# Kernel optimization log

Measured on AMD Instinct MI355X. Metric: run time of the kernel, lower is better.

The kernel has to match this reference:

```python
import jax, jax.numpy as jnp
import numpy as np

B, L, C = 4, 8192, 256
HEADS = 1
DP = C // HEADS
FFN_HID = C * 2 * 4  # (d_model*2) * ffn_dim_expansion
EPS = 1e-5


def _layernorm(x, gamma, beta):
    mu = jnp.mean(x, axis=-1, keepdims=True)
    var = jnp.var(x, axis=-1, keepdims=True)
    return (x - mu) * jax.lax.rsqrt(var + EPS) * gamma + beta


def setup_inputs() -> dict:
    key = jax.random.key(0)
    ks = jax.random.split(key, 12)
    s = 0.02
    return {
        "source": jax.random.normal(ks[0], (B, L, C), jnp.float32),
        "target": jax.random.normal(ks[1], (B, L, C), jnp.float32),
        "Wq": jax.random.normal(ks[2], (C, C), jnp.float32) * s,
        "Wk": jax.random.normal(ks[3], (C, C), jnp.float32) * s,
        "Wv": jax.random.normal(ks[4], (C, C), jnp.float32) * s,
        "Wl": jax.random.normal(ks[5], (C, C), jnp.float32) * s,
        "gamma1": jnp.ones((C,), jnp.float32),
        "beta1": jnp.zeros((C,), jnp.float32),
        "W1": jax.random.normal(ks[6], (2 * C, FFN_HID), jnp.float32) * s,
        "b1": jnp.zeros((FFN_HID,), jnp.float32),
        "W2": jax.random.normal(ks[7], (FFN_HID, C), jnp.float32) * s,
        "b2": jnp.zeros((C,), jnp.float32),
        "gamma2": jnp.ones((C,), jnp.float32),
        "beta2": jnp.zeros((C,), jnp.float32),
        "h": 64,
        "w": 128,
    }


def reference(source, target, Wq, Wk, Wv, Wl, gamma1, beta1, W1, b1, W2, b2,
              gamma2, beta2, h, w):
    assert L == h * w
    q = (source @ Wq).reshape(B, L, HEADS, DP)
    k = (target @ Wk).reshape(B, L, HEADS, DP)
    v = (target @ Wv).reshape(B, L, HEADS, DP)
    k = jax.nn.softmax(k, axis=1)  # softmax over token dim
    context = jnp.einsum('bnhd,bnhe->bhde', q, k)   # small d×d per head
    attn = jnp.einsum('bhde,bnhe->bnhd', context, v).reshape(B, L, C)
    message = _layernorm(attn @ Wl, gamma1, beta1)
    hidden = jax.nn.gelu(jnp.concatenate([source, message], axis=-1) @ W1 + b1,
                         approximate=False)
    message = _layernorm(hidden @ W2 + b2, gamma2, beta2)
    return source + message
```

## Files before the change

kernel.cpp:

```cpp
#include <hip/hip_runtime.h>
#include <hip/hip_bf16.h>

typedef unsigned short u16;
typedef __attribute__((ext_vector_type(8))) short short8;
typedef __attribute__((ext_vector_type(4))) float f32x4;

#define B_    4
#define L_    8192
#define C_    256
#define BL_   (B_*L_)
#define BLC_  (BL_*C_)
#define FFN_  2048
#define KCAT_ 512
#define EPS_  1e-5f

__device__ __forceinline__ float bf2f(u16 v) {
  union { unsigned int u; float f; } x; x.u = ((unsigned int)v) << 16; return x.f;
}
__device__ __forceinline__ u16 f2bf(float f) {
  union { float f; unsigned int u; } x; x.f = f;
  unsigned int lsb = (x.u >> 16) & 1u;
  return (u16)((x.u + 0x7fffu + lsb) >> 16);
}
__device__ __forceinline__ float gelu_f(float x) {
  float z = fabsf(x) * 0.70710678118654752f;
  float t = __builtin_amdgcn_rcpf(1.f + 0.3275911f * z);
  float p = ((((1.061405429f * t - 1.453152027f) * t + 1.421413741f) * t
              - 0.284496736f) * t + 0.254829592f) * t;
  float e = __expf(-z * z);
  float erfv = copysignf(1.f - p * e, x);
  return 0.5f * x * (1.f + erfv);
}

template<int MODE, int ACT, int SPLITK>
__launch_bounds__(256, 2)
__global__ void gemm_abt(const u16* __restrict__ A0, const u16* __restrict__ A1,
                         int SEL, int lda,
                         const u16* __restrict__ Bt,
                         const float* __restrict__ bias,
                         u16* __restrict__ Cb, float* __restrict__ Cf,
                         int M, int N, int K,
                         long sAb, long sBb, long sCb)
{
  __shared__ __align__(16) u16 As[2 * 128 * 32];
  __shared__ __align__(16) u16 Bs[2 * 128 * 32];

  const int ntiles = N >> 7;
  const int tile = blockIdx.x;
  const int mt0 = (tile / ntiles) << 7;
  const int nt0 = (tile % ntiles) << 7;
  const int kchunk = K / (int)gridDim.y;
  const int k0beg = blockIdx.y * kchunk;
  const int k0end = k0beg + kchunk;
  const int bz = blockIdx.z;
  A0 += (long)bz * sAb;  A1 += (long)bz * sAb;  Bt += (long)bz * sBb;

  const u16* Abase = (MODE == 2 && nt0 >= SEL) ? A1 : A0;

  const int tid  = threadIdx.x;
  const int wave = tid >> 6, lane = tid & 63;
  const int srow = lane >> 2;
  const int cq   = lane & 3;
  const int gq   = cq ^ (srow & 3);
  const int frow = lane & 15;
  const int fq   = lane >> 4;
  const int fqx  = (fq ^ (frow & 3)) * 8;

  f32x4 zero = {0.f, 0.f, 0.f, 0.f};
  f32x4 acc[4][4];
#pragma unroll
  for (int i = 0; i < 4; i++)
#pragma unroll
    for (int j = 0; j < 4; j++) acc[i][j] = zero;

  const int wm = (wave & 1) * 64, wn = (wave >> 1) * 64;

  for (int k0 = k0beg; k0 < k0end; k0 += 64) {
    __syncthreads();
    const u16* Asrc;
    int ka;
    if (MODE == 1) {
      const bool lo = (k0 < SEL);
      Asrc = lo ? A0 : A1;
      ka = lo ? k0 : (k0 - SEL);
    } else { Asrc = Abase; ka = k0; }

#pragma unroll
    for (int h = 0; h < 2; h++) {
#pragma unroll
      for (int i = 0; i < 2; i++) {
        const int chunk = i * 4 + wave;
        const u16* ga = Asrc + (long)(mt0 + chunk * 16 + srow) * lda
                        + (ka + h * 32 + gq * 8);
        __builtin_amdgcn_global_load_lds(
            (const __attribute__((address_space(1))) unsigned int*)ga,
            (__attribute__((address_space(3))) unsigned int*)&As[h * 4096 + chunk * 16 * 32],
            16, 0, 0);
        const u16* gb = Bt + (long)(nt0 + chunk * 16 + srow) * K
                        + (k0 + h * 32 + gq * 8);
        __builtin_amdgcn_global_load_lds(
            (const __attribute__((address_space(1))) unsigned int*)gb,
            (__attribute__((address_space(3))) unsigned int*)&Bs[h * 4096 + chunk * 16 * 32],
            16, 0, 0);
      }
    }
    __syncthreads();

#pragma unroll
    for (int h = 0; h < 2; h++) {
      short8 af[4], bf[4];
#pragma unroll
      for (int t = 0; t < 4; t++)
        af[t] = *(const short8*)&As[h * 4096 + (wm + t * 16 + frow) * 32 + fqx];
#pragma unroll
      for (int t = 0; t < 4; t++)
        bf[t] = *(const short8*)&Bs[h * 4096 + (wn + t * 16 + frow) * 32 + fqx];
#pragma unroll
      for (int mt = 0; mt < 4; mt++)
#pragma unroll
        for (int nt = 0; nt < 4; nt++)
          acc[mt][nt] = __builtin_amdgcn_mfma_f32_16x16x32_bf16(af[mt], bf[nt], acc[mt][nt], 0, 0, 0);
    }
  }

  if (SPLITK) {
    float* Cp = Cf + (long)bz * sCb;
#pragma unroll
    for (int mt = 0; mt < 4; mt++)
#pragma unroll
      for (int r = 0; r < 4; r++) {
        const int row = mt0 + wm + mt * 16 + fq * 4 + r;
#pragma unroll
        for (int nt = 0; nt < 4; nt++) {
          const int col = nt0 + wn + nt * 16 + frow;
          atomicAdd(&Cp[(long)row * N + col], acc[mt][nt][r]);
        }
      }
  } else {
    u16* Cp = Cb + (long)bz * sCb;
    float bv[4];
#pragma unroll
    for (int nt = 0; nt < 4; nt++)
      bv[nt] = bias ? bias[nt0 + wn + nt * 16 + frow] : 0.f;
#pragma unroll
    for (int mt = 0; mt < 4; mt++)
#pragma unroll
      for (int r = 0; r < 4; r++) {
        const int row = mt0 + wm + mt * 16 + fq * 4 + r;
#pragma unroll
        for (int nt = 0; nt < 4; nt++) {
          const int col = nt0 + wn + nt * 16 + frow;
          float v = acc[mt][nt][r] + bv[nt];
          if (ACT == 1) v = gelu_f(v);
          Cp[(long)row * N + col] = f2bf(v);
        }
      }
  }
}

__global__ void transpose2d(const u16* __restrict__ in, u16* __restrict__ out,
                            int R, int Cc, int ldi, long sIb, long sOb)
{
  __shared__ u16 t[32][33];
  const int bx = blockIdx.x * 32;
  const int by = blockIdx.y * 32;
  in  += (long)blockIdx.z * sIb;
  out += (long)blockIdx.z * sOb;
  const int tx = threadIdx.x, ty = threadIdx.y;
#pragma unroll
  for (int i = ty; i < 32; i += 8)
    t[i][tx] = in[(long)(by + i) * ldi + bx + tx];
  __syncthreads();
#pragma unroll
  for (int i = ty; i < 32; i += 8)
    out[(long)(bx + i) * R + by + tx] = t[tx][i];
}

__global__ void transpose_f2b(const float* __restrict__ in, u16* __restrict__ out,
                              int R, int Cc)
{
  __shared__ u16 t[32][33];
  const int bx = blockIdx.x * 32;
  const int by = blockIdx.y * 32;
  const int tx = threadIdx.x, ty = threadIdx.y;
#pragma unroll
  for (int i = ty; i < 32; i += 8)
    t[i][tx] = f2bf(in[(long)(by + i) * Cc + bx + tx]);
  __syncthreads();
#pragma unroll
  for (int i = ty; i < 32; i += 8)
    out[(long)(bx + i) * R + by + tx] = t[tx][i];
}

__global__ void pack_w256(const float* __restrict__ w0, const float* __restrict__ w1,
                          const float* __restrict__ w2, const float* __restrict__ w3,
                          u16* __restrict__ qkvT, u16* __restrict__ wlT)
{
  __shared__ u16 t[32][33];
  const int z = blockIdx.z;
  const float* in = (z == 0) ? w0 : (z == 1) ? w1 : (z == 2) ? w2 : w3;
  u16* out = (z < 3) ? (qkvT + (long)z * C_ * C_) : wlT;
  const int bx = blockIdx.x * 32, by = blockIdx.y * 32;
  const int tx = threadIdx.x, ty = threadIdx.y;
#pragma unroll
  for (int i = ty; i < 32; i += 8)
    t[i][tx] = f2bf(in[(long)(by + i) * C_ + bx + tx]);
  __syncthreads();
#pragma unroll
  for (int i = ty; i < 32; i += 8)
    out[(long)(bx + i) * C_ + by + tx] = t[tx][i];
}

__global__ void cast2_f2b(const float* __restrict__ in0, const float* __restrict__ in1,
                          u16* __restrict__ out0, u16* __restrict__ out1)
{
  const float* in = blockIdx.y ? in1 : in0;
  u16* out = blockIdx.y ? out1 : out0;
  int i = (blockIdx.x * 256 + threadIdx.x) * 4;
  float4 v = *(const float4*)(in + i);
  ushort4 o; o.x = f2bf(v.x); o.y = f2bf(v.y); o.z = f2bf(v.z); o.w = f2bf(v.w);
  *(ushort4*)(out + i) = o;
}

__global__ void softmax_rows(u16* __restrict__ data, int rowlen)
{
  const long base = (long)blockIdx.x * rowlen;
  const int tid = threadIdx.x, wave = tid >> 6, lane = tid & 63;
  __shared__ float red[4];

  float m = -3.4e38f;
  for (int i = tid; i < rowlen; i += 256) m = fmaxf(m, bf2f(data[base + i]));
#pragma unroll
  for (int off = 32; off; off >>= 1) m = fmaxf(m, __shfl_xor(m, off, 64));
  if (lane == 0) red[wave] = m;
  __syncthreads();
  m = fmaxf(fmaxf(red[0], red[1]), fmaxf(red[2], red[3]));
  __syncthreads();

  float s = 0.f;
  for (int i = tid; i < rowlen; i += 256) s += expf(bf2f(data[base + i]) - m);
#pragma unroll
  for (int off = 32; off; off >>= 1) s += __shfl_xor(s, off, 64);
  if (lane == 0) red[wave] = s;
  __syncthreads();
  const float inv = 1.f / (red[0] + red[1] + red[2] + red[3]);
  for (int i = tid; i < rowlen; i += 256)
    data[base + i] = f2bf(expf(bf2f(data[base + i]) - m) * inv);
}

template<int OUTF>
__global__ void layernorm_rows(const u16* __restrict__ x,
                               const float* __restrict__ gamma,
                               const float* __restrict__ beta,
                               const float* __restrict__ src,
                               void* __restrict__ outv)
{
  const int wave = threadIdx.x >> 6, lane = threadIdx.x & 63;
  const long row = (long)blockIdx.x * 4 + wave;
  ushort4 raw = ((const ushort4*)(x + row * C_))[lane];
  float v0 = bf2f(raw.x), v1 = bf2f(raw.y), v2 = bf2f(raw.z), v3 = bf2f(raw.w);
  float s = v0 + v1 + v2 + v3;
  float q = v0 * v0 + v1 * v1 + v2 * v2 + v3 * v3;
#pragma unroll
  for (int off = 32; off; off >>= 1) {
    s += __shfl_xor(s, off, 64);
    q += __shfl_xor(q, off, 64);
  }
  const float mu  = s * (1.f / C_);
  const float var = q * (1.f / C_) - mu * mu;
  const float rs  = 1.f / sqrtf(var + EPS_);
  float4 gr = ((const float4*)gamma)[lane];
  float4 br = ((const float4*)beta)[lane];
  float o0 = (v0 - mu) * rs * gr.x + br.x;
  float o1 = (v1 - mu) * rs * gr.y + br.y;
  float o2 = (v2 - mu) * rs * gr.z + br.z;
  float o3 = (v3 - mu) * rs * gr.w + br.w;
  if (OUTF) {
    float4 sr = ((const float4*)(src + row * C_))[lane];
    float4 ow; ow.x = o0 + sr.x; ow.y = o1 + sr.y; ow.z = o2 + sr.z; ow.w = o3 + sr.w;
    ((float4*)((float*)outv + row * C_))[lane] = ow;
  } else {
    ushort4 ow; ow.x = f2bf(o0); ow.y = f2bf(o1); ow.z = f2bf(o2); ow.w = f2bf(o3);
    ((ushort4*)((u16*)outv + row * C_))[lane] = ow;
  }
}

__global__ void zero_f32(float* __restrict__ p, int n) {
  int i = blockIdx.x * 256 + threadIdx.x;
  if (i < n) p[i] = 0.f;
}
__global__ void f32_to_bf16_k(const float* __restrict__ in, u16* __restrict__ out, int n) {
  int i = blockIdx.x * 256 + threadIdx.x;
  if (i < n) out[i] = f2bf(in[i]);
}

extern "C" void kernel_launch(void* const* d_in, const int* in_sizes, int n_in,
                              void* d_out, int out_size, void* d_ws, size_t ws_size,
                              hipStream_t stream)
{
  const float* source = (const float*)d_in[0];
  const float* target = (const float*)d_in[1];
  const float* Wq     = (const float*)d_in[2];
  const float* Wk     = (const float*)d_in[3];
  const float* Wv     = (const float*)d_in[4];
  const float* Wl     = (const float*)d_in[5];
  const float* gamma1 = (const float*)d_in[6];
  const float* beta1  = (const float*)d_in[7];
  const float* W1     = (const float*)d_in[8];
  const float* b1     = (const float*)d_in[9];
  const float* W2     = (const float*)d_in[10];
  const float* b2     = (const float*)d_in[11];
  const float* gamma2 = (const float*)d_in[12];
  const float* beta2  = (const float*)d_in[13];
  (void)in_sizes; (void)n_in; (void)out_size;

  char* ws = (char*)d_ws;
  size_t off = 0;
  auto take = [&](size_t bytes) -> char* {
    char* p = ws + off; off += (bytes + 255) & ~(size_t)255; return p;
  };
  u16*   WqkvT = (u16*)take((size_t)768 * C_ * 2);
  u16*   WlT   = (u16*)take((size_t)C_ * C_ * 2);
  u16*   W1T   = (u16*)take((size_t)FFN_ * KCAT_ * 2);
  u16*   W2T   = (u16*)take((size_t)C_ * FFN_ * 2);
  float* ctxTf = (float*)take((size_t)B_ * C_ * C_ * 4);
  u16*   ctxTb = (u16*)take((size_t)B_ * C_ * C_ * 2);
  u16*   Mtb   = (u16*)take((size_t)B_ * C_ * C_ * 2);
  u16*   srcB  = (u16*)take((size_t)BLC_ * 2);
  u16*   bufB  = (u16*)take((size_t)BLC_ * 2);
  u16*   bufD  = (u16*)take((size_t)BLC_ * 2);
  u16*   bufE  = (u16*)take((size_t)BLC_ * 2);
  const size_t ubase = off;
  u16* tgtB = (u16*)(ws + ubase);
  u16* QKV  = (u16*)(ws + ubase + (size_t)BLC_ * 2);
  u16* qT   = (u16*)(ws + ubase + (size_t)BLC_ * 2 + (size_t)BL_ * 768 * 2);
  u16* kT   = qT + (size_t)BLC_;
  const size_t live = (size_t)BLC_ * 2 * 3 + (size_t)BL_ * 768 * 2;
  int nchunk = 1;
  while (nchunk < 16) {
    size_t hid = (size_t)(BL_ / nchunk) * FFN_ * 2;
    size_t need = ubase + (hid > live ? hid : live);
    if (need <= ws_size) break;
    nchunk <<= 1;
  }
  const int Mc = BL_ / nchunk;
  u16* hidden = (u16*)(ws + ubase);

  dim3 tb(32, 8);
  cast2_f2b<<<dim3(BLC_ / 1024, 2), 256, 0, stream>>>(source, target, srcB, tgtB);
  pack_w256<<<dim3(8, 8, 4), tb, 0, stream>>>(Wq, Wk, Wv, Wl, WqkvT, WlT);
  transpose_f2b<<<dim3(FFN_/32, KCAT_/32), tb, 0, stream>>>(W1, W1T, KCAT_, FFN_);
  transpose_f2b<<<dim3(C_/32,  FFN_/32), tb, 0, stream>>>(W2, W2T, FFN_, C_);
  zero_f32<<<(B_*C_*C_)/256, 256, 0, stream>>>(ctxTf, B_*C_*C_);

  gemm_abt<2,0,0><<<dim3((BL_/128)*(768/128)), 256, 0, stream>>>(
      srcB, tgtB, 256, C_, WqkvT, nullptr, QKV, nullptr, BL_, 768, C_, 0, 0, 0);

  transpose2d<<<dim3(C_/32, L_/32, B_), tb, 0, stream>>>(QKV,       qT, L_, C_, 768, (long)L_*768, (long)L_*C_);
  transpose2d<<<dim3(C_/32, L_/32, B_), tb, 0, stream>>>(QKV + 256, kT, L_, C_, 768, (long)L_*768, (long)L_*C_);
  softmax_rows<<<B_*C_, 256, 0, stream>>>(kT, L_);

  gemm_abt<0,0,1><<<dim3(4, 16, B_), 256, 0, stream>>>(
      kT, kT, 0, L_, qT, nullptr, nullptr, ctxTf, C_, C_, L_,
      (long)C_*L_, (long)C_*L_, (long)C_*C_);
  f32_to_bf16_k<<<(B_*C_*C_)/256, 256, 0, stream>>>(ctxTf, ctxTb, B_*C_*C_);

  gemm_abt<0,0,0><<<dim3(4, 1, B_), 256, 0, stream>>>(
      WlT, WlT, 0, C_, ctxTb, nullptr, Mtb, nullptr, C_, C_, C_,
      0, (long)C_*C_, (long)C_*C_);

  gemm_abt<0,0,0><<<dim3((L_/128)*(C_/128), 1, B_), 256, 0, stream>>>(
      QKV + 512, QKV + 512, 0, 768, Mtb, nullptr, bufB, nullptr, L_, C_, C_,
      (long)L_*768, (long)C_*C_, (long)L_*C_);

  layernorm_rows<0><<<BL_/4, 256, 0, stream>>>(bufB, gamma1, beta1, nullptr, bufD);

  for (int ch = 0; ch < nchunk; ch++) {
    const long moff = (long)ch * Mc;
    gemm_abt<1,1,0><<<dim3((Mc/128)*(FFN_/128)), 256, 0, stream>>>(
        srcB + moff * C_, bufD + moff * C_, C_, C_, W1T, b1, hidden, nullptr,
        Mc, FFN_, KCAT_, 0, 0, 0);
    gemm_abt<0,0,0><<<dim3((Mc/128)*(C_/128)), 256, 0, stream>>>(
        hidden, hidden, 0, FFN_, W2T, b2, bufE + moff * C_, nullptr,
        Mc, C_, FFN_, 0, 0, 0);
  }

  layernorm_rows<1><<<BL_/4, 256, 0, stream>>>(bufE, gamma2, beta2, source, d_out);
}
```

Before: 420.3 us.

## Fuse attention-out GEMM with LayerNorm and fuse whole FFN into one kernel

Replaces the attn@Wl GEMM plus separate LayerNorm with a gemm_ln kernel that computes 64x256 row tiles and applies LayerNorm in the epilogue. The two FFN GEMMs, GELU, bias, LayerNorm2 and the residual add move into one ffn_fused kernel that keeps the hidden activations in LDS per 128-column slice, so the large hidden buffer never goes through HBM. This removes the intermediate memory traffic and several launches. The cost is lower tile reuse with 64-row tiles, many more synchronisations, and W1/W2 being reread for every row block. The generic GEMM also switches to M-major tile ordering.

```diff
diff --git a/kernel.cpp b/kernel.cpp
--- a/kernel.cpp
+++ b/kernel.cpp
@@ -14,6 +14,10 @@
 #define KCAT_ 512
 #define EPS_  1e-5f
 
+#define GLDS(dst, src) __builtin_amdgcn_global_load_lds( \
+    (const __attribute__((address_space(1))) unsigned int*)(src), \
+    (__attribute__((address_space(3))) unsigned int*)(dst), 16, 0, 0)
+
 __device__ __forceinline__ float bf2f(u16 v) {
   union { unsigned int u; float f; } x; x.u = ((unsigned int)v) << 16; return x.f;
 }
@@ -32,12 +36,11 @@
   return 0.5f * x * (1.f + erfv);
 }
 
-template<int MODE, int ACT, int SPLITK>
+template<int MODE, int SPLITK>
 __launch_bounds__(256, 2)
 __global__ void gemm_abt(const u16* __restrict__ A0, const u16* __restrict__ A1,
                          int SEL, int lda,
                          const u16* __restrict__ Bt,
-                         const float* __restrict__ bias,
                          u16* __restrict__ Cb, float* __restrict__ Cf,
                          int M, int N, int K,
                          long sAb, long sBb, long sCb)
@@ -45,10 +48,10 @@
   __shared__ __align__(16) u16 As[2 * 128 * 32];
   __shared__ __align__(16) u16 Bs[2 * 128 * 32];
 
-  const int ntiles = N >> 7;
+  const int mtiles = M >> 7;
   const int tile = blockIdx.x;
-  const int mt0 = (tile / ntiles) << 7;
-  const int nt0 = (tile % ntiles) << 7;
+  const int mt0 = (tile % mtiles) << 7;
+  const int nt0 = (tile / mtiles) << 7;
   const int kchunk = K / (int)gridDim.y;
   const int k0beg = blockIdx.y * kchunk;
   const int k0end = k0beg + kchunk;
@@ -60,8 +63,7 @@
   const int tid  = threadIdx.x;
   const int wave = tid >> 6, lane = tid & 63;
   const int srow = lane >> 2;
-  const int cq   = lane & 3;
-  const int gq   = cq ^ (srow & 3);
+  const int gq   = (lane & 3) ^ (srow & 3);
   const int frow = lane & 15;
   const int fq   = lane >> 4;
   const int fqx  = (fq ^ (frow & 3)) * 8;
@@ -77,35 +79,18 @@
 
   for (int k0 = k0beg; k0 < k0end; k0 += 64) {
     __syncthreads();
-    const u16* Asrc;
-    int ka;
-    if (MODE == 1) {
-      const bool lo = (k0 < SEL);
-      Asrc = lo ? A0 : A1;
-      ka = lo ? k0 : (k0 - SEL);
-    } else { Asrc = Abase; ka = k0; }
-
 #pragma unroll
     for (int h = 0; h < 2; h++) {
 #pragma unroll
       for (int i = 0; i < 2; i++) {
         const int chunk = i * 4 + wave;
-        const u16* ga = Asrc + (long)(mt0 + chunk * 16 + srow) * lda
-                        + (ka + h * 32 + gq * 8);
-        __builtin_amdgcn_global_load_lds(
-            (const __attribute__((address_space(1))) unsigned int*)ga,
-            (__attribute__((address_space(3))) unsigned int*)&As[h * 4096 + chunk * 16 * 32],
-            16, 0, 0);
-        const u16* gb = Bt + (long)(nt0 + chunk * 16 + srow) * K
-                        + (k0 + h * 32 + gq * 8);
-        __builtin_amdgcn_global_load_lds(
-            (const __attribute__((address_space(1))) unsigned int*)gb,
-            (__attribute__((address_space(3))) unsigned int*)&Bs[h * 4096 + chunk * 16 * 32],
-            16, 0, 0);
+        GLDS(&As[h * 4096 + chunk * 512],
+             Abase + (long)(mt0 + chunk * 16 + srow) * lda + (k0 + h * 32 + gq * 8));
+        GLDS(&Bs[h * 4096 + chunk * 512],
+             Bt + (long)(nt0 + chunk * 16 + srow) * K + (k0 + h * 32 + gq * 8));
       }
     }
     __syncthreads();
-
 #pragma unroll
     for (int h = 0; h < 2; h++) {
       short8 af[4], bf[4];
@@ -131,39 +116,292 @@
       for (int r = 0; r < 4; r++) {
         const int row = mt0 + wm + mt * 16 + fq * 4 + r;
 #pragma unroll
-        for (int nt = 0; nt < 4; nt++) {
-          const int col = nt0 + wn + nt * 16 + frow;
-          atomicAdd(&Cp[(long)row * N + col], acc[mt][nt][r]);
-        }
+        for (int nt = 0; nt < 4; nt++)
+          atomicAdd(&Cp[(long)row * N + nt0 + wn + nt * 16 + frow], acc[mt][nt][r]);
       }
   } else {
     u16* Cp = Cb + (long)bz * sCb;
-    float bv[4];
-#pragma unroll
-    for (int nt = 0; nt < 4; nt++)
-      bv[nt] = bias ? bias[nt0 + wn + nt * 16 + frow] : 0.f;
 #pragma unroll
     for (int mt = 0; mt < 4; mt++)
 #pragma unroll
       for (int r = 0; r < 4; r++) {
         const int row = mt0 + wm + mt * 16 + fq * 4 + r;
 #pragma unroll
-        for (int nt = 0; nt < 4; nt++) {
-          const int col = nt0 + wn + nt * 16 + frow;
-          float v = acc[mt][nt][r] + bv[nt];
-          if (ACT == 1) v = gelu_f(v);
-          Cp[(long)row * N + col] = f2bf(v);
+        for (int nt = 0; nt < 4; nt++)
+          Cp[(long)row * N + nt0 + wn + nt * 16 + frow] = f2bf(acc[mt][nt][r]);
+      }
+  }
+}
+
+__launch_bounds__(256, 2)
+__global__ void gemm_ln(const u16* __restrict__ A, long sAb, int lda,
+                        const u16* __restrict__ Bt, long sBb,
+                        const float* __restrict__ gamma, const float* __restrict__ beta,
+                        u16* __restrict__ outb)
+{
+  __shared__ __align__(16) u16 As[2 * 64 * 32];
+  __shared__ __align__(16) u16 Bs[2 * 256 * 32];
+  __shared__ float red_s[64][4], red_q[64][4];
+
+  const int gm0 = blockIdx.x * 64;
+  const int z  = gm0 >> 13;
+  const int ml = gm0 & (L_ - 1);
+  A  += (long)z * sAb + (long)ml * lda;
+  Bt += (long)z * sBb;
+
+  const int tid = threadIdx.x, wave = tid >> 6, lane = tid & 63;
+  const int srow = lane >> 2, gq = (lane & 3) ^ (srow & 3);
+  const int frow = lane & 15, fq = lane >> 4;
+  const int fqx = (fq ^ (frow & 3)) * 8;
+  const int wn = wave * 64;
+
+  f32x4 zero = {0.f, 0.f, 0.f, 0.f};
+  f32x4 acc[4][4];
+#pragma unroll
+  for (int i = 0; i < 4; i++)
+#pragma unroll
+    for (int j = 0; j < 4; j++) acc[i][j] = zero;
+
+  for (int k0 = 0; k0 < 256; k0 += 64) {
+    __syncthreads();
+#pragma unroll
+    for (int h = 0; h < 2; h++) {
+      GLDS(&As[h * 2048 + wave * 512],
+           A + (long)(wave * 16 + srow) * lda + (k0 + h * 32 + gq * 8));
+#pragma unroll
+      for (int i = 0; i < 4; i++) {
+        const int chunk = i * 4 + wave;
+        GLDS(&Bs[h * 8192 + chunk * 512],
+             Bt + (long)(chunk * 16 + srow) * 256 + (k0 + h * 32 + gq * 8));
+      }
+    }
+    __syncthreads();
+#pragma unroll
+    for (int h = 0; h < 2; h++) {
+      short8 af[4], bf[4];
+#pragma unroll
+      for (int t = 0; t < 4; t++)
+        af[t] = *(const short8*)&As[h * 2048 + (t * 16 + frow) * 32 + fqx];
+#pragma unroll
+      for (int t = 0; t < 4; t++)
+        bf[t] = *(const short8*)&Bs[h * 8192 + (wn + t * 16 + frow) * 32 + fqx];
+#pragma unroll
+      for (int mt = 0; mt < 4; mt++)
+#pragma unroll
+        for (int nt = 0; nt < 4; nt++)
+          acc[mt][nt] = __builtin_amdgcn_mfma_f32_16x16x32_bf16(af[mt], bf[nt], acc[mt][nt], 0, 0, 0);
+    }
+  }
+
+  float gv[4], bv[4];
+#pragma unroll
+  for (int nt = 0; nt < 4; nt++) {
+    const int col = wn + nt * 16 + frow;
+    gv[nt] = gamma[col]; bv[nt] = beta[col];
+  }
+#pragma unroll
+  for (int mt = 0; mt < 4; mt++)
+#pragma unroll
+    for (int r = 0; r < 4; r++) {
+      float s = 0.f, q = 0.f;
+#pragma unroll
+      for (int nt = 0; nt < 4; nt++) {
+        float v = acc[mt][nt][r]; s += v; q += v * v;
+      }
+#pragma unroll
+      for (int m = 1; m < 16; m <<= 1) {
+        s += __shfl_xor(s, m, 16); q += __shfl_xor(q, m, 16);
+      }
+      if (frow == 0) {
+        const int row = mt * 16 + fq * 4 + r;
+        red_s[row][wave] = s; red_q[row][wave] = q;
+      }
+    }
+  __syncthreads();
+#pragma unroll
+  for (int mt = 0; mt < 4; mt++)
+#pragma unroll
+    for (int r = 0; r < 4; r++) {
+      const int row = mt * 16 + fq * 4 + r;
+      float4 ss = *(const float4*)red_s[row];
+      float4 qq = *(const float4*)red_q[row];
+      const float s = ss.x + ss.y + ss.z + ss.w;
+      const float q = qq.x + qq.y + qq.z + qq.w;
+      const float mu = s * (1.f / 256.f);
+      const float var = q * (1.f / 256.f) - mu * mu;
+      const float rs = 1.f / sqrtf(var + EPS_);
+      const long grow = gm0 + row;
+#pragma unroll
+      for (int nt = 0; nt < 4; nt++) {
+        const int col = wn + nt * 16 + frow;
+        outb[grow * 256 + col] = f2bf((acc[mt][nt][r] - mu) * rs * gv[nt] + bv[nt]);
+      }
+    }
+}
+
+__launch_bounds__(256, 2)
+__global__ void ffn_fused(const u16* __restrict__ srcB, const u16* __restrict__ message,
+                          const u16* __restrict__ W1T, const float* __restrict__ b1,
+                          const u16* __restrict__ W2T, const float* __restrict__ b2,
+                          const float* __restrict__ gamma2, const float* __restrict__ beta2,
+                          const float* __restrict__ source, float* __restrict__ out)
+{
+  __shared__ __align__(16) u16 As[2 * 64 * 32];
+  __shared__ __align__(16) u16 Bs1[2 * 128 * 32];
+  __shared__ __align__(16) u16 Bs2[2 * 256 * 32];
+  __shared__ __align__(16) u16 Hs[64 * 136];
+  __shared__ float red_s[64][4], red_q[64][4];
+
+  const int m0 = blockIdx.x * 64;
+  const int tid = threadIdx.x, wave = tid >> 6, lane = tid & 63;
+  const int srow = lane >> 2, gq = (lane & 3) ^ (srow & 3);
+  const int frow = lane & 15, fq = lane >> 4;
+  const int fqx = (fq ^ (frow & 3)) * 8;
+  const int wn1 = wave * 32;
+  const int wn2 = wave * 64;
+
+  f32x4 zero = {0.f, 0.f, 0.f, 0.f};
+  f32x4 acc2[4][4];
+#pragma unroll
+  for (int i = 0; i < 4; i++)
+#pragma unroll
+    for (int j = 0; j < 4; j++) acc2[i][j] = zero;
+
+  for (int hs = 0; hs < 16; hs++) {
+    f32x4 acc1[4][2];
+#pragma unroll
+    for (int i = 0; i < 4; i++) { acc1[i][0] = zero; acc1[i][1] = zero; }
+
+    for (int it = 0; it < 8; it++) {
+      const int k0 = it * 64;
+      const u16* Asrc = (k0 < 256) ? srcB : message;
+      const int ka = k0 & 255;
+      __syncthreads();
+#pragma unroll
+      for (int h = 0; h < 2; h++) {
+        GLDS(&As[h * 2048 + wave * 512],
+             Asrc + (long)(m0 + wave * 16 + srow) * 256 + (ka + h * 32 + gq * 8));
+#pragma unroll
+        for (int i = 0; i < 2; i++) {
+          const int chunk = i * 4 + wave;
+          GLDS(&Bs1[h * 4096 + chunk * 512],
+               W1T + (long)(hs * 128 + chunk * 16 + srow) * 512 + (k0 + h * 32 + gq * 8));
         }
       }
+      __syncthreads();
+#pragma unroll
+      for (int h = 0; h < 2; h++) {
+        short8 af[4], bf[2];
+#pragma unroll
+        for (int t = 0; t < 4; t++)
+          af[t] = *(const short8*)&As[h * 2048 + (t * 16 + frow) * 32 + fqx];
+#pragma unroll
+        for (int t = 0; t < 2; t++)
+          bf[t] = *(const short8*)&Bs1[h * 4096 + (wn1 + t * 16 + frow) * 32 + fqx];
+#pragma unroll
+        for (int mt = 0; mt < 4; mt++)
+#pragma unroll
+          for (int nt = 0; nt < 2; nt++)
+            acc1[mt][nt] = __builtin_amdgcn_mfma_f32_16x16x32_bf16(af[mt], bf[nt], acc1[mt][nt], 0, 0, 0);
+      }
+    }
+    float b1v[2];
+#pragma unroll
+    for (int nt = 0; nt < 2; nt++)
+      b1v[nt] = b1[hs * 128 + wn1 + nt * 16 + frow];
+#pragma unroll
+    for (int mt = 0; mt < 4; mt++)
+#pragma unroll
+      for (int nt = 0; nt < 2; nt++)
+#pragma unroll
+        for (int r = 0; r < 4; r++) {
+          const int row = mt * 16 + fq * 4 + r;
+          Hs[row * 136 + wn1 + nt * 16 + frow] = f2bf(gelu_f(acc1[mt][nt][r] + b1v[nt]));
+        }
+
+    for (int it2 = 0; it2 < 2; it2++) {
+      __syncthreads();
+#pragma unroll
+      for (int h = 0; h < 2; h++)
+#pragma unroll
+        for (int i = 0; i < 4; i++) {
+          const int chunk = i * 4 + wave;
+          GLDS(&Bs2[h * 8192 + chunk * 512],
+               W2T + (long)(chunk * 16 + srow) * 2048
+                   + (hs * 128 + it2 * 64 + h * 32 + gq * 8));
+        }
+      __syncthreads();
+#pragma unroll
+      for (int kk = 0; kk < 2; kk++) {
+        short8 a2[4], b2f[4];
+#pragma unroll
+        for (int t = 0; t < 4; t++)
+          a2[t] = *(const short8*)&Hs[(t * 16 + frow) * 136 + it2 * 64 + kk * 32 + fq * 8];
+#pragma unroll
+        for (int t = 0; t < 4; t++)
+          b2f[t] = *(const short8*)&Bs2[kk * 8192 + (wn2 + t * 16 + frow) * 32 + fqx];
+#pragma unroll
+        for (int mt = 0; mt < 4; mt++)
+#pragma unroll
+          for (int nt = 0; nt < 4; nt++)
+            acc2[mt][nt] = __builtin_amdgcn_mfma_f32_16x16x32_bf16(a2[mt], b2f[nt], acc2[mt][nt], 0, 0, 0);
+      }
+    }
   }
+
+  float b2v[4], gv[4], bv[4];
+#pragma unroll
+  for (int nt = 0; nt < 4; nt++) {
+    const int col = wn2 + nt * 16 + frow;
+    b2v[nt] = b2[col]; gv[nt] = gamma2[col]; bv[nt] = beta2[col];
+  }
+#pragma unroll
+  for (int mt = 0; mt < 4; mt++)
+#pragma unroll
+    for (int r = 0; r < 4; r++) {
+      float s = 0.f, q = 0.f;
+#pragma unroll
+      for (int nt = 0; nt < 4; nt++) {
+        float v = acc2[mt][nt][r] + b2v[nt];
+        acc2[mt][nt][r] = v; s += v; q += v * v;
+      }
+#pragma unroll
+      for (int m = 1; m < 16; m <<= 1) {
+        s += __shfl_xor(s, m, 16); q += __shfl_xor(q, m, 16);
+      }
+      if (frow == 0) {
+        const int row = mt * 16 + fq * 4 + r;
+        red_s[row][wave] = s; red_q[row][wave] = q;
+      }
+    }
+  __syncthreads();
+#pragma unroll
+  for (int mt = 0; mt < 4; mt++)
+#pragma unroll
+    for (int r = 0; r < 4; r++) {
+      const int row = mt * 16 + fq * 4 + r;
+      float4 ss = *(const float4*)red_s[row];
+      float4 qq = *(const float4*)red_q[row];
+      const float s = ss.x + ss.y + ss.z + ss.w;
+      const float q = qq.x + qq.y + qq.z + qq.w;
+      const float mu = s * (1.f / 256.f);
+      const float var = q * (1.f / 256.f) - mu * mu;
+      const float rs = 1.f / sqrtf(var + EPS_);
+      const long grow = m0 + row;
+#pragma unroll
+      for (int nt = 0; nt < 4; nt++) {
+        const int col = wn2 + nt * 16 + frow;
+        out[grow * 256 + col] = (acc2[mt][nt][r] - mu) * rs * gv[nt] + bv[nt]
+                                + source[grow * 256 + col];
+      }
+    }
 }
 
 __global__ void transpose2d(const u16* __restrict__ in, u16* __restrict__ out,
                             int R, int Cc, int ldi, long sIb, long sOb)
 {
   __shared__ u16 t[32][33];
-  const int bx = blockIdx.x * 32;
-  const int by = blockIdx.y * 32;
+  const int bx = blockIdx.x * 32, by = blockIdx.y * 32;
   in  += (long)blockIdx.z * sIb;
   out += (long)blockIdx.z * sOb;
   const int tx = threadIdx.x, ty = threadIdx.y;
@@ -180,8 +418,7 @@
                               int R, int Cc)
 {
   __shared__ u16 t[32][33];
-  const int bx = blockIdx.x * 32;
-  const int by = blockIdx.y * 32;
+  const int bx = blockIdx.x * 32, by = blockIdx.y * 32;
   const int tx = threadIdx.x, ty = threadIdx.y;
 #pragma unroll
   for (int i = ty; i < 32; i += 8)
@@ -246,43 +483,6 @@
   const float inv = 1.f / (red[0] + red[1] + red[2] + red[3]);
   for (int i = tid; i < rowlen; i += 256)
     data[base + i] = f2bf(expf(bf2f(data[base + i]) - m) * inv);
-}
-
-template<int OUTF>
-__global__ void layernorm_rows(const u16* __restrict__ x,
-                               const float* __restrict__ gamma,
-                               const float* __restrict__ beta,
-                               const float* __restrict__ src,
-                               void* __restrict__ outv)
-{
-  const int wave = threadIdx.x >> 6, lane = threadIdx.x & 63;
-  const long row = (long)blockIdx.x * 4 + wave;
-  ushort4 raw = ((const ushort4*)(x + row * C_))[lane];
-  float v0 = bf2f(raw.x), v1 = bf2f(raw.y), v2 = bf2f(raw.z), v3 = bf2f(raw.w);
-  float s = v0 + v1 + v2 + v3;
-  float q = v0 * v0 + v1 * v1 + v2 * v2 + v3 * v3;
-#pragma unroll
-  for (int off = 32; off; off >>= 1) {
-    s += __shfl_xor(s, off, 64);
-    q += __shfl_xor(q, off, 64);
-  }
-  const float mu  = s * (1.f / C_);
-  const float var = q * (1.f / C_) - mu * mu;
-  const float rs  = 1.f / sqrtf(var + EPS_);
-  float4 gr = ((const float4*)gamma)[lane];
-  float4 br = ((const float4*)beta)[lane];
-  float o0 = (v0 - mu) * rs * gr.x + br.x;
-  float o1 = (v1 - mu) * rs * gr.y + br.y;
-  float o2 = (v2 - mu) * rs * gr.z + br.z;
-  float o3 = (v3 - mu) * rs * gr.w + br.w;
-  if (OUTF) {
-    float4 sr = ((const float4*)(src + row * C_))[lane];
-    float4 ow; ow.x = o0 + sr.x; ow.y = o1 + sr.y; ow.z = o2 + sr.z; ow.w = o3 + sr.w;
-    ((float4*)((float*)outv + row * C_))[lane] = ow;
-  } else {
-    ushort4 ow; ow.x = f2bf(o0); ow.y = f2bf(o1); ow.z = f2bf(o2); ow.w = f2bf(o3);
-    ((ushort4*)((u16*)outv + row * C_))[lane] = ow;
-  }
 }
 
 __global__ void zero_f32(float* __restrict__ p, int n) {
@@ -312,7 +512,7 @@
   const float* b2     = (const float*)d_in[11];
   const float* gamma2 = (const float*)d_in[12];
   const float* beta2  = (const float*)d_in[13];
-  (void)in_sizes; (void)n_in; (void)out_size;
+  (void)in_sizes; (void)n_in; (void)out_size; (void)ws_size;
 
   char* ws = (char*)d_ws;
   size_t off = 0;
@@ -327,24 +527,11 @@
   u16*   ctxTb = (u16*)take((size_t)B_ * C_ * C_ * 2);
   u16*   Mtb   = (u16*)take((size_t)B_ * C_ * C_ * 2);
   u16*   srcB  = (u16*)take((size_t)BLC_ * 2);
-  u16*   bufB  = (u16*)take((size_t)BLC_ * 2);
-  u16*   bufD  = (u16*)take((size_t)BLC_ * 2);
-  u16*   bufE  = (u16*)take((size_t)BLC_ * 2);
-  const size_t ubase = off;
-  u16* tgtB = (u16*)(ws + ubase);
-  u16* QKV  = (u16*)(ws + ubase + (size_t)BLC_ * 2);
-  u16* qT   = (u16*)(ws + ubase + (size_t)BLC_ * 2 + (size_t)BL_ * 768 * 2);
-  u16* kT   = qT + (size_t)BLC_;
-  const size_t live = (size_t)BLC_ * 2 * 3 + (size_t)BL_ * 768 * 2;
-  int nchunk = 1;
-  while (nchunk < 16) {
-    size_t hid = (size_t)(BL_ / nchunk) * FFN_ * 2;
-    size_t need = ubase + (hid > live ? hid : live);
-    if (need <= ws_size) break;
-    nchunk <<= 1;
-  }
-  const int Mc = BL_ / nchunk;
-  u16* hidden = (u16*)(ws + ubase);
+  u16*   tgtB  = (u16*)take((size_t)BLC_ * 2);
+  u16*   QKV   = (u16*)take((size_t)BL_ * 768 * 2);
+  u16*   qT    = (u16*)take((size_t)BLC_ * 2);
+  u16*   kT    = (u16*)take((size_t)BLC_ * 2);
+  u16*   msg   = (u16*)take((size_t)BLC_ * 2);
 
   dim3 tb(32, 8);
   cast2_f2b<<<dim3(BLC_ / 1024, 2), 256, 0, stream>>>(source, target, srcB, tgtB);
@@ -353,37 +540,25 @@
   transpose_f2b<<<dim3(C_/32,  FFN_/32), tb, 0, stream>>>(W2, W2T, FFN_, C_);
   zero_f32<<<(B_*C_*C_)/256, 256, 0, stream>>>(ctxTf, B_*C_*C_);
 
-  gemm_abt<2,0,0><<<dim3((BL_/128)*(768/128)), 256, 0, stream>>>(
-      srcB, tgtB, 256, C_, WqkvT, nullptr, QKV, nullptr, BL_, 768, C_, 0, 0, 0);
+  gemm_abt<2,0><<<dim3((BL_/128)*(768/128)), 256, 0, stream>>>(
+      srcB, tgtB, 256, C_, WqkvT, QKV, nullptr, BL_, 768, C_, 0, 0, 0);
 
   transpose2d<<<dim3(C_/32, L_/32, B_), tb, 0, stream>>>(QKV,       qT, L_, C_, 768, (long)L_*768, (long)L_*C_);
   transpose2d<<<dim3(C_/32, L_/32, B_), tb, 0, stream>>>(QKV + 256, kT, L_, C_, 768, (long)L_*768, (long)L_*C_);
   softmax_rows<<<B_*C_, 256, 0, stream>>>(kT, L_);
 
-  gemm_abt<0,0,1><<<dim3(4, 16, B_), 256, 0, stream>>>(
-      kT, kT, 0, L_, qT, nullptr, nullptr, ctxTf, C_, C_, L_,
+  gemm_abt<0,1><<<dim3(4, 16, B_), 256, 0, stream>>>(
+      kT, kT, 0, L_, qT, nullptr, ctxTf, C_, C_, L_,
       (long)C_*L_, (long)C_*L_, (long)C_*C_);
   f32_to_bf16_k<<<(B_*C_*C_)/256, 256, 0, stream>>>(ctxTf, ctxTb, B_*C_*C_);
 
-  gemm_abt<0,0,0><<<dim3(4, 1, B_), 256, 0, stream>>>(
-      WlT, WlT, 0, C_, ctxTb, nullptr, Mtb, nullptr, C_, C_, C_,
+  gemm_abt<0,0><<<dim3(4, 1, B_), 256, 0, stream>>>(
+      WlT, WlT, 0, C_, ctxTb, Mtb, nullptr, C_, C_, C_,
       0, (long)C_*C_, (long)C_*C_);
 
-  gemm_abt<0,0,0><<<dim3((L_/128)*(C_/128), 1, B_), 256, 0, stream>>>(
-      QKV + 512, QKV + 512, 0, 768, Mtb, nullptr, bufB, nullptr, L_, C_, C_,
-      (long)L_*768, (long)C_*C_, (long)L_*C_);
-
-  layernorm_rows<0><<<BL_/4, 256, 0, stream>>>(bufB, gamma1, beta1, nullptr, bufD);
-
-  for (int ch = 0; ch < nchunk; ch++) {
-    const long moff = (long)ch * Mc;
-    gemm_abt<1,1,0><<<dim3((Mc/128)*(FFN_/128)), 256, 0, stream>>>(
-        srcB + moff * C_, bufD + moff * C_, C_, C_, W1T, b1, hidden, nullptr,
-        Mc, FFN_, KCAT_, 0, 0, 0);
-    gemm_abt<0,0,0><<<dim3((Mc/128)*(C_/128)), 256, 0, stream>>>(
-        hidden, hidden, 0, FFN_, W2T, b2, bufE + moff * C_, nullptr,
-        Mc, C_, FFN_, 0, 0, 0);
-  }
-
-  layernorm_rows<1><<<BL_/4, 256, 0, stream>>>(bufE, gamma2, beta2, source, d_out);
-}
+  gemm_ln<<<BL_/64, 256, 0, stream>>>(
+      QKV + 512, (long)L_*768, 768, Mtb, (long)C_*C_, gamma1, beta1, msg);
+
+  ffn_fused<<<BL_/64, 256, 0, stream>>>(
+      srcB, msg, W1T, b1, W2T, b2, gamma2, beta2, source, (float*)d_out);
+}
```

New measurement: 449.5 us. +6.9%, slower.
